# Kernel optimization log

Measured on AMD Instinct MI355X. Metric: run time of the kernel, lower is better.

The kernel has to match this reference:

```python
import jax, jax.numpy as jnp
import numpy as np
import math

B, S, D, H, DFF, V = 8, 512, 512, 8, 2048, 32000
EPS = 1e-5

def _pe_table(max_len, d):
    pos = jnp.arange(max_len, dtype=jnp.float32)[:, None]
    i = jnp.arange(d)
    exponent = (2 * (i // 2)).astype(jnp.float32) / d
    angle = pos / jnp.power(10000.0, exponent)[None, :]
    return jnp.where(i % 2 == 0, jnp.sin(angle), jnp.cos(angle))

def _ln(x, g, b):
    mu = jnp.mean(x, -1, keepdims=True)
    var = jnp.mean((x - mu) ** 2, -1, keepdims=True)
    return g * (x - mu) * jax.lax.rsqrt(var + EPS) + b

def setup_inputs() -> dict:
    key = jax.random.key(0)
    ks = jax.random.split(key, 16)
    n = jax.random.normal
    return {
        "tokens": jax.random.randint(ks[0], (B, S), 0, V, dtype=jnp.int32),
        "emb": n(ks[1], (V, D), jnp.float32),
        "pe": _pe_table(1000, D),
        "Wq": n(ks[2], (H, D, D), jnp.float32), "bq": jnp.zeros((H, D), jnp.float32),
        "Wk": n(ks[3], (H, D, D), jnp.float32), "bk": jnp.zeros((H, D), jnp.float32),
        "Wv": n(ks[4], (H, D, D), jnp.float32), "bv": jnp.zeros((H, D), jnp.float32),
        "Wo": n(ks[5], (H * D, D), jnp.float32), "bo": jnp.zeros((D,), jnp.float32),
        "g1": jnp.ones((D,), jnp.float32), "be1": jnp.zeros((D,), jnp.float32),
        "W1": n(ks[6], (D, DFF), jnp.float32), "b1": jnp.zeros((DFF,), jnp.float32),
        "W2": n(ks[7], (DFF, D), jnp.float32), "b2": jnp.zeros((D,), jnp.float32),
        "g2": jnp.ones((D,), jnp.float32), "be2": jnp.zeros((D,), jnp.float32),
        "Wf": n(ks[8], (D, V), jnp.float32), "bf": jnp.zeros((V,), jnp.float32),
    }

def reference(tokens, emb, pe, Wq, bq, Wk, bk, Wv, bv, Wo, bo, g1, be1,
              W1, b1, W2, b2, g2, be2, Wf, bf):
    x = emb[tokens] + pe[:tokens.shape[1]]  # [B,S,D]
    res = x
    # input-level "causal" mask over (seq, feature) plane, as in the source
    mask = jnp.triu(jnp.ones((S, D), dtype=bool), k=1)
    xm = jnp.where(mask, 0.0, x)
    scale = 1.0 / math.sqrt(D)
    q = jnp.einsum('bsd,hde->hbse', xm, Wq) + bq[:, None, None, :]
    k = jnp.einsum('bsd,hde->hbse', xm, Wk) + bk[:, None, None, :]
    v = jnp.einsum('bsd,hde->hbse', xm, Wv) + bv[:, None, None, :]
    attn = jax.nn.softmax(jnp.einsum('hbse,hbte->hbst', q, k) * scale, axis=-1)
    o = jnp.einsum('hbst,hbte->hbse', attn, v)  # [H,B,S,D]
    cat = o.transpose(1, 2, 0, 3).reshape(B, S, H * D)  # matches torch.cat head order
    x = _ln(res + (cat @ Wo + bo), g1, be1)
    res = x
    ff = jax.nn.relu(x @ W1 + b1) @ W2 + b2
    x = _ln(res + ff, g2, be2)
    return x @ Wf + bf  # [B,S,V]
```

## Files before the change

### kernel.cpp

```cpp
#include <hip/hip_runtime.h>

typedef unsigned short u16;
typedef unsigned int u32;
typedef short s16x8 __attribute__((ext_vector_type(8)));
typedef __bf16 bf16x8 __attribute__((ext_vector_type(8)));
typedef float f32x4 __attribute__((ext_vector_type(4)));

#define DEVI static __device__ __forceinline__

#define SS 512
#define DD 512
#define NFF 2048
#define VV 32000
#define MTOT 4096
#define HD 4096
#define KC 1536

DEVI float bf2f(u16 h){ return __uint_as_float(((u32)h) << 16); }
DEVI u16 f2bf(float f){
  u32 u = __float_as_uint(f);
  return (u16)((u + 0x7FFFu + ((u >> 16) & 1u)) >> 16);
}
DEVI float ldf(const void* p, long i, int isbf){
  return isbf ? bf2f(((const u16*)p)[i]) : ((const float*)p)[i];
}

DEVI f32x4 mfma16(s16x8 a, s16x8 b, f32x4 c){
  return __builtin_amdgcn_mfma_f32_16x16x32_bf16(
      __builtin_bit_cast(bf16x8, a), __builtin_bit_cast(bf16x8, b), c, 0, 0, 0);
}

typedef const __attribute__((address_space(1))) unsigned int* gup;
typedef __attribute__((address_space(3))) unsigned int* lup;
DEVI void gload16(const void* g, void* l){
  __builtin_amdgcn_global_load_lds((gup)g, (lup)l, 16, 0, 0);
}

DEVI float wave_redmax(float v){
  #pragma unroll
  for (int off = 32; off > 0; off >>= 1) v = fmaxf(v, __shfl_xor(v, off, 64));
  return v;
}
DEVI float wave_redsum(float v){
  #pragma unroll
  for (int off = 32; off > 0; off >>= 1) v += __shfl_xor(v, off, 64);
  return v;
}

__global__ void k_dflag(const void* pe, int* flag){
  flag[0] = (*(const u32*)pe == 0x3F800000u) ? 1 : 0;
}

__global__ __launch_bounds__(256) void k_embed(
    const int* __restrict__ tok, const void* __restrict__ emb, const void* __restrict__ pe,
    float* __restrict__ x, u16* __restrict__ xm2, const int* __restrict__ dflag)
{
  int isbf = dflag[0];
  int blk = blockIdx.x;
  int s = blk & (SS - 1);
  int t = tok[blk];
  long rb = (long)blk * 1024;
  for (int d = threadIdx.x; d < DD; d += 256){
    float e = ldf(emb, (long)t * DD + d, isbf) + ldf(pe, (long)s * DD + d, isbf);
    x[(long)blk * DD + d] = e;
    float m = (d <= s) ? e : 0.f;
    u16 hi = f2bf(m);
    u16 lo = f2bf(m - bf2f(hi));
    xm2[rb + d] = hi;
    xm2[rb + 512 + d] = lo;
  }
}

__global__ __launch_bounds__(256) void k_wsplitT(
    const void* __restrict__ Wq, const void* __restrict__ Wk,
    u16* __restrict__ Wq2, u16* __restrict__ Wk2, const int* __restrict__ dflag)
{
  int isbf = dflag[0];
  int zz = blockIdx.z;
  const void* in = (zz < 8) ? Wq : Wk;
  u16* out = (zz < 8) ? Wq2 : Wk2;
  int z = zz & 7;
  long zin = (long)z * DD * DD;
  long zout = (long)z * DD * 1024;
  __shared__ float t[32][33];
  int e0 = blockIdx.x * 32, d0 = blockIdx.y * 32;
  int tx = threadIdx.x & 31, ty = threadIdx.x >> 5;
  #pragma unroll
  for (int i = 0; i < 4; i++){
    int d = ty + i * 8;
    t[d][tx] = ldf(in, zin + (long)(d0 + d) * DD + e0 + tx, isbf);
  }
  __syncthreads();
  #pragma unroll
  for (int i = 0; i < 4; i++){
    int e = ty + i * 8;
    float v = t[tx][e];
    u16 hi = f2bf(v);
    u16 lo = f2bf(v - bf2f(hi));
    long ob = zout + (long)(e0 + e) * 1024 + d0 + tx;
    out[ob] = hi;
    out[ob + 512] = lo;
  }
}

__global__ __launch_bounds__(256) void k_transAll(
    const void* __restrict__ Wv, const void* __restrict__ Wo,
    const void* __restrict__ W1, const void* __restrict__ W2,
    const void* __restrict__ Wf,
    u16* __restrict__ WvT, u16* __restrict__ WoT, u16* __restrict__ W1T,
    u16* __restrict__ W2T, u16* __restrict__ WfT, const int* __restrict__ dflag)
{
  int isbf = dflag[0];
  int f = blockIdx.x;
  const void* in; u16* out; int R, C, gx, loc;
  if (f < 2048)      { in = Wv; out = WvT; R = 512;  C = 512;   gx = 16;   loc = f; }
  else if (f < 4096) { in = Wo; out = WoT; R = 4096; C = 512;   gx = 16;   loc = f - 2048; }
  else if (f < 5120) { in = W1; out = W1T; R = 512;  C = 2048;  gx = 64;   loc = f - 4096; }
  else if (f < 6144) { in = W2; out = W2T; R = 2048; C = 512;   gx = 16;   loc = f - 5120; }
  else               { in = Wf; out = WfT; R = 512;  C = 32000; gx = 1000; loc = f - 6144; }
  int bx = loc % gx;
  int rest = loc / gx;
  int gy = R >> 5;
  int by = rest % gy, z = rest / gy;
  long zo = (long)z * R * C;
  __shared__ float t[32][33];
  int c0 = bx * 32, r0 = by * 32;
  int tx = threadIdx.x & 31, ty = threadIdx.x >> 5;
  #pragma unroll
  for (int i = 0; i < 4; i++){
    int r = ty + i * 8;
    t[r][tx] = ldf(in, zo + (long)(r0 + r) * C + c0 + tx, isbf);
  }
  __syncthreads();
  #pragma unroll
  for (int i = 0; i < 4; i++){
    int c = ty + i * 8;
    out[zo + (long)(c0 + c) * R + r0 + tx] = f2bf(t[tx][c]);
  }
}

enum { EP_QK = 0, EP_SCALE = 1, EP_VT = 2, EP_CAT = 3, EP_OUT = 4,
       EP_F32RES = 5, EP_RELU = 6 };

template<int MODE, bool GSWAP>
__global__ __launch_bounds__(256) void k_mfma(
    const u16* __restrict__ A, long sA, int lda,
    const u16* __restrict__ Bt, long sB,
    void* __restrict__ Cv,
    const void* __restrict__ bias,
    const float* __restrict__ res,
    int K, int ldc, float scale,
    const int* __restrict__ dflag)
{
  int isbf = dflag[0];
  int z = blockIdx.z;
  const u16* Ab = A + (long)z * sA;
  const u16* Bb = Bt + (long)z * sB;
  __shared__ __align__(16) u16 As[2][4][128][8];
  __shared__ __align__(16) u16 Bs[2][4][128][8];
  int m0 = (GSWAP ? blockIdx.x : blockIdx.y) * 128;
  int n0 = (GSWAP ? blockIdx.y : blockIdx.x) * 128;
  int tid = threadIdx.x;
  int lane = tid & 63, w = tid >> 6;
  int wr = (w >> 1) * 64, wc = (w & 1) * 64;
  int l15 = lane & 15, l4 = lane >> 4;
  int s0 = w * 64 + lane;
  int ar0 = s0 & 127, ak0 = s0 >> 7;
  int ak1 = ak0 + 2;
  f32x4 zero = {0.f, 0.f, 0.f, 0.f};
  f32x4 acc[4][4];
  #pragma unroll
  for (int i = 0; i < 4; i++)
    #pragma unroll
    for (int j = 0; j < 4; j++) acc[i][j] = zero;

  const long arow0 = (long)(m0 + ar0) * lda;
  const long brow0 = (long)(n0 + ar0) * K;

  #define STAGE(buf, k0) do{ \
    u16* AsF = &As[buf][0][0][0]; \
    u16* BsF = &Bs[buf][0][0][0]; \
    gload16(Ab + arow0 + (k0) + ak0 * 8, AsF + (long)(w * 64) * 8); \
    gload16(Ab + arow0 + (k0) + ak1 * 8, AsF + (long)(256 + w * 64) * 8); \
    gload16(Bb + brow0 + (k0) + ak0 * 8, BsF + (long)(w * 64) * 8); \
    gload16(Bb + brow0 + (k0) + ak1 * 8, BsF + (long)(256 + w * 64) * 8); \
  }while(0)

  #define COMPUTE(buf) do{ \
    s16x8 af[4], bfr[4]; \
    _Pragma("unroll") \
    for (int i = 0; i < 4; i++) af[i] = *(const s16x8*)&As[buf][l4][wr + i * 16 + l15][0]; \
    _Pragma("unroll") \
    for (int j = 0; j < 4; j++) bfr[j] = *(const s16x8*)&Bs[buf][l4][wc + j * 16 + l15][0]; \
    _Pragma("unroll") \
    for (int i = 0; i < 4; i++) \
      _Pragma("unroll") \
      for (int j = 0; j < 4; j++) \
        acc[i][j] = mfma16(af[i], bfr[j], acc[i][j]); \
  }while(0)

  STAGE(0, 0);
  __syncthreads();
  for (int k0 = 0; k0 < K; k0 += 64){
    STAGE(1, k0 + 32);
    COMPUTE(0);
    __syncthreads();
    if (k0 + 64 < K) STAGE(0, k0 + 64);
    COMPUTE(1);
    __syncthreads();
  }
  #undef STAGE
  #undef COMPUTE

  int mbase = m0 + wr + l4 * 4;
  int nbase = n0 + wc + l15;
  if constexpr (MODE == EP_F32RES){
    float* C = (float*)Cv;
    #pragma unroll
    for (int j = 0; j < 4; j++){
      int n = nbase + j * 16;
      float badd = ldf(bias, n, isbf);
      #pragma unroll
      for (int i = 0; i < 4; i++)
        #pragma unroll
        for (int r = 0; r < 4; r++){
          long a = (long)(mbase + i * 16 + r) * ldc + n;
          C[a] = acc[i][j][r] + badd + res[a];
        }
    }
  } else if constexpr (MODE == EP_RELU){
    u16* C = (u16*)Cv;
    #pragma unroll
    for (int j = 0; j < 4; j++){
      int n = nbase + j * 16;
      float badd = ldf(bias, n, isbf);
      #pragma unroll
      for (int i = 0; i < 4; i++)
        #pragma unroll
        for (int r = 0; r < 4; r++)
          C[(long)(mbase + i * 16 + r) * ldc + n] = f2bf(fmaxf(acc[i][j][r] + badd, 0.f));
    }
  }
}

template<int MODE, bool GSWAP, int AMAP, int BMAP>
__global__ __launch_bounds__(512, 2) void k_mfma2(
    const u16* __restrict__ A, long sA, int lda,
    const u16* __restrict__ Bt, long sB, int ldb,
    void* __restrict__ Cv,
    const void* __restrict__ bias,
    const float* __restrict__ res,
    int K, int ldc, float scale,
    const int* __restrict__ dflag)
{
  int isbf = dflag[0];
  int z = blockIdx.z;
  const u16* Ab = A + (long)z * sA;
  const u16* Bb = Bt + (long)z * sB;
  __shared__ __align__(16) char smem[65536];
  u16* SA = (u16*)smem;
  u16* SB = (u16*)(smem + 32768);
  int m0 = (GSWAP ? blockIdx.x : blockIdx.y) * 256;
  int n0 = (GSWAP ? blockIdx.y : blockIdx.x) * 256;
  int tid = threadIdx.x;
  int lane = tid & 63, w = tid >> 6;
  int wm = (w >> 2) * 128, wn = (w & 3) * 64;
  int l15 = lane & 15, l4 = lane >> 4;
  int row = tid & 255, ob = tid >> 8;
  f32x4 zero = {0.f, 0.f, 0.f, 0.f};
  f32x4 acc[8][4];
  #pragma unroll
  for (int i = 0; i < 8; i++)
    #pragma unroll
    for (int j = 0; j < 4; j++) acc[i][j] = zero;

  const long arow0 = (long)(m0 + row) * lda;
  const long brow0 = (long)(n0 + row) * ldb;

  #define STAGE2(buf, k0_) do{ \
    int ka = (AMAP == 1) ? ((k0_) < 512 ? (k0_) : (k0_) - 512) \
           : (AMAP == 2) ? ((k0_) < 1024 ? (k0_) : (k0_) - 1024) : (k0_); \
    int kb = (BMAP == 1) ? ((k0_) < 512 ? (k0_) : (k0_) - 512) \
           : (BMAP == 2) ? ((k0_) < 1024 ? (k0_) : (k0_) - 1024) : (k0_); \
    gload16(Ab + arow0 + ka + ob * 8,       SA + ((buf) * 8192 + (ob * 256 + row) * 8)); \
    gload16(Ab + arow0 + ka + (ob + 2) * 8, SA + ((buf) * 8192 + ((ob + 2) * 256 + row) * 8)); \
    gload16(Bb + brow0 + kb + ob * 8,       SB + ((buf) * 8192 + (ob * 256 + row) * 8)); \
    gload16(Bb + brow0 + kb + (ob + 2) * 8, SB + ((buf) * 8192 + ((ob + 2) * 256 + row) * 8)); \
  }while(0)

  #define COMPUTE2(buf) do{ \
    s16x8 bfr[4]; \
    _Pragma("unroll") \
    for (int j = 0; j < 4; j++) \
      bfr[j] = *(const s16x8*)(SB + ((buf) * 8192 + l4 * 2048 + (wn + j * 16 + l15) * 8)); \
    _Pragma("unroll") \
    for (int i = 0; i < 8; i++){ \
      s16x8 af = *(const s16x8*)(SA + ((buf) * 8192 + l4 * 2048 + (wm + i * 16 + l15) * 8)); \
      _Pragma("unroll") \
      for (int j = 0; j < 4; j++) \
        acc[i][j] = mfma16(af, bfr[j], acc[i][j]); \
    } \
  }while(0)

  STAGE2(0, 0);
  __syncthreads();
  for (int k0 = 0; k0 < K; k0 += 64){
    STAGE2(1, k0 + 32);
    COMPUTE2(0);
    __syncthreads();
    if (k0 + 64 < K) STAGE2(0, k0 + 64);
    COMPUTE2(1);
    __syncthreads();
  }
  #undef STAGE2
  #undef COMPUTE2

  int mbase = m0 + wm + l4 * 4;
  int nbase = n0 + wn + l15;
  if constexpr (MODE == EP_QK){
    u16* C = (u16*)Cv + (long)z * ((long)MTOT * 1024);
    #pragma unroll
    for (int j = 0; j < 4; j++){
      int n = nbase + j * 16;
      float badd = ldf(bias, (long)z * DD + n, isbf);
      #pragma unroll
      for (int i = 0; i < 8; i++)
        #pragma unroll
        for (int r = 0; r < 4; r++){
          float qv = acc[i][j][r] + badd;
          u16 hi = f2bf(qv);
          u16 lo = f2bf(qv - bf2f(hi));
          long rb = (long)(mbase + i * 16 + r) * 1024;
          C[rb + n] = hi;
          C[rb + 512 + n] = lo;
        }
    }
  } else if constexpr (MODE == EP_SCALE){
    float* C = (float*)Cv + (long)z * SS * SS;
    #pragma unroll
    for (int i = 0; i < 8; i++)
      #pragma unroll
      for (int j = 0; j < 4; j++)
        #pragma unroll
        for (int r = 0; r < 4; r++)
          C[(long)(mbase + i * 16 + r) * SS + nbase + j * 16] = acc[i][j][r] * scale;
  } else if constexpr (MODE == EP_VT){
    u16* C = (u16*)Cv;
    #pragma unroll
    for (int i = 0; i < 8; i++){
      int mrow = mbase + i * 16;
      int b = mrow >> 9, s = mrow & (SS - 1);
      #pragma unroll
      for (int j = 0; j < 4; j++){
        int n = nbase + j * 16;
        float badd = ldf(bias, (long)z * DD + n, isbf);
        ushort4 pk;
        pk.x = f2bf(acc[i][j][0] + badd); pk.y = f2bf(acc[i][j][1] + badd);
        pk.z = f2bf(acc[i][j][2] + badd); pk.w = f2bf(acc[i][j][3] + badd);
        *(ushort4*)&C[((long)(z * 8 + b) * DD + n) * SS + s] = pk;
      }
    }
  } else if constexpr (MODE == EP_CAT){
    u16* C = (u16*)Cv;
    int h = z >> 3, b = z & 7;
    #pragma unroll
    for (int i = 0; i < 8; i++){
      int s = mbase + i * 16;
      #pragma unroll
      for (int j = 0; j < 4; j++){
        int n = nbase + j * 16;
        #pragma unroll
        for (int r = 0; r < 4; r++)
          C[((long)b * SS + s + r) * HD + (long)h * DD + n] = f2bf(acc[i][j][r]);
      }
    }
  } else if constexpr (MODE == EP_OUT){
    float* O = (float*)Cv;
    float* ldsT = (float*)smem;
    const int RST = 260;
    int hs16 = (w >> 2) * 16;
    float badd[4];
    #pragma unroll
    for (int j = 0; j < 4; j++) badd[j] = ldf(bias, n0 + wn + j * 16 + l15, isbf);
    #pragma unroll
    for (int i = 0; i < 8; i++){
      __syncthreads();
      #pragma unroll
      for (int j = 0; j < 4; j++){
        int col = wn + j * 16 + l15;
        #pragma unroll
        for (int r = 0; r < 4; r++)
          ldsT[(hs16 + l4 * 4 + r) * RST + col] = acc[i][j][r] + badd[j];
      }
      __syncthreads();
      #pragma unroll
      for (int p = 0; p < 4; p++){
        int chunk = tid + p * 512;
        int lr = chunk >> 6, c4 = chunk & 63;
        int gm = m0 + (lr >> 4) * 128 + i * 16 + (lr & 15);
        float4 v = *(float4*)&ldsT[lr * RST + c4 * 4];
        *(float4*)&O[(long)gm * ldc + n0 + c4 * 4] = v;
      }
    }
  }
}

__global__ __launch_bounds__(256) void k_softmax(const float* __restrict__ S, u16* __restrict__ P)
{
  int row = blockIdx.x * 4 + (threadIdx.x >> 6);
  int lane = threadIdx.x & 63;
  const float* p = S + (long)row * SS + lane * 8;
  float4 v0 = *(const float4*)p;
  float4 v1 = *(const float4*)(p + 4);
  float v[8] = {v0.x, v0.y, v0.z, v0.w, v1.x, v1.y, v1.z, v1.w};
  float mx = v[0];
  #pragma unroll
  for (int i = 1; i < 8; i++) mx = fmaxf(mx, v[i]);
  mx = wave_redmax(mx);
  float e[8], sum = 0.f;
  #pragma unroll
  for (int i = 0; i < 8; i++){ e[i] = expf(v[i] - mx); sum += e[i]; }
  sum = wave_redsum(sum);
  float inv = 1.f / sum;
  u16* q = P + (long)row * SS + lane * 8;
  ushort4 o0, o1;
  o0.x = f2bf(e[0] * inv); o0.y = f2bf(e[1] * inv);
  o0.z = f2bf(e[2] * inv); o0.w = f2bf(e[3] * inv);
  o1.x = f2bf(e[4] * inv); o1.y = f2bf(e[5] * inv);
  o1.z = f2bf(e[6] * inv); o1.w = f2bf(e[7] * inv);
  *(ushort4*)q = o0;
  *(ushort4*)(q + 4) = o1;
}

template<bool WF32>
__global__ __launch_bounds__(256) void k_ln(
    const float* __restrict__ X, const void* __restrict__ g, const void* __restrict__ be,
    u16* __restrict__ Yb, float* __restrict__ Yf, const int* __restrict__ dflag)
{
  int isbf = dflag[0];
  int row = blockIdx.x * 4 + (threadIdx.x >> 6);
  int lane = threadIdx.x & 63;
  const float* p = X + (long)row * DD + lane * 8;
  float4 v0 = *(const float4*)p;
  float4 v1 = *(const float4*)(p + 4);
  float v[8] = {v0.x, v0.y, v0.z, v0.w, v1.x, v1.y, v1.z, v1.w};
  float s = 0.f;
  #pragma unroll
  for (int i = 0; i < 8; i++) s += v[i];
  s = wave_redsum(s);
  float mu = s * (1.f / DD);
  float d_[8], sq = 0.f;
  #pragma unroll
  for (int i = 0; i < 8; i++){ d_[i] = v[i] - mu; sq += d_[i] * d_[i]; }
  sq = wave_redsum(sq);
  float rs = 1.f / sqrtf(sq * (1.f / DD) + 1e-5f);
  #pragma unroll
  for (int i = 0; i < 8; i++){
    int dd = lane * 8 + i;
    float y = ldf(g, dd, isbf) * d_[i] * rs + ldf(be, dd, isbf);
    Yb[(long)row * DD + dd] = f2bf(y);
    if (WF32) Yf[(long)row * DD + dd] = y;
  }
}

extern "C" void kernel_launch(void* const* d_in, const int* in_sizes, int n_in,
                              void* d_out, int out_size, void* d_ws, size_t ws_size,
                              hipStream_t stream)
{
  const int* tokens = (const int*)d_in[0];
  const void* emb = d_in[1];
  const void* pe  = d_in[2];
  const void* Wq  = d_in[3];
  const void* bq  = d_in[4];
  const void* Wk  = d_in[5];
  const void* bk  = d_in[6];
  const void* Wv  = d_in[7];
  const void* bv  = d_in[8];
  const void* Wo  = d_in[9];
  const void* bo  = d_in[10];
  const void* g1  = d_in[11];
  const void* be1 = d_in[12];
  const void* W1  = d_in[13];
  const void* b1  = d_in[14];
  const void* W2  = d_in[15];
  const void* b2  = d_in[16];
  const void* g2  = d_in[17];
  const void* be2 = d_in[18];
  const void* Wf  = d_in[19];
  const void* bfb = d_in[20];
  float* out = (float*)d_out;
  char* ws = (char*)d_ws;
  char* DO = (char*)d_out;

  const size_t MB = 1ull << 20;
  int* dflag = (int*)ws;
  u16* x2b   = (u16*)(ws + 1 * MB);
  u16* WfT   = (u16*)(ws + 8 * MB);

  float* x    = (float*)(DO + 0 * MB);
  u16*   xm2  = (u16*)(DO + 8 * MB);
  u16*   Wq2  = (u16*)(DO + 16 * MB);
  u16*   Wk2  = (u16*)(DO + 24 * MB);
  u16*   WvT  = (u16*)(DO + 32 * MB);
  u16*   WoT  = (u16*)(DO + 36 * MB);
  u16*   W1T  = (u16*)(DO + 40 * MB);
  u16*   W2T  = (u16*)(DO + 42 * MB);
  u16*   q2   = (u16*)(DO + 48 * MB);
  u16*   k2   = (u16*)(DO + 112 * MB);
  float* sc   = (float*)(DO + 176 * MB);
  u16*   attn = (u16*)(DO + 240 * MB);
  u16*   vT   = (u16*)(DO + 272 * MB);
  u16*   cat  = (u16*)(DO + 304 * MB);
  float* proj = (float*)(DO + 336 * MB);
  float* x1f  = (float*)(DO + 344 * MB);
  u16*   x1b  = (u16*)(DO + 352 * MB);
  u16*   ff1  = (u16*)(DO + 356 * MB);
  float* ff2  = (float*)(DO + 372 * MB);

  const float scale = 0.04419417382415922f;
  const long HSL = 262144;
  const long WSL = 524288;
  const long QSL = 524288;

  k_dflag<<<1, 1, 0, stream>>>(pe, dflag);
  k_embed<<<dim3(4096), 256, 0, stream>>>(tokens, emb, pe, x, xm2, dflag);

  k_wsplitT<<<dim3(16, 16, 16), 256, 0, stream>>>(Wq, Wk, Wq2, Wk2, dflag);
  k_transAll<<<dim3(22144), 256, 0, stream>>>(
      Wv, Wo, W1, W2, Wf, WvT, WoT, W1T, W2T, WfT, dflag);

  k_mfma2<EP_QK, false, 1, 2><<<dim3(2, 16, 8), 512, 0, stream>>>(
      xm2, 0, 1024, Wq2, WSL, 1024, q2, bq, nullptr, KC, 0, 0.f, dflag);
  k_mfma2<EP_QK, false, 1, 2><<<dim3(2, 16, 8), 512, 0, stream>>>(
      xm2, 0, 1024, Wk2, WSL, 1024, k2, bk, nullptr, KC, 0, 0.f, dflag);
  k_mfma2<EP_VT, false, 0, 0><<<dim3(2, 16, 8), 512, 0, stream>>>(
      xm2, 0, 1024, WvT, HSL, 512, vT, bv, nullptr, DD, 0, 0.f, dflag);

  k_mfma2<EP_SCALE, false, 1, 2><<<dim3(2, 2, 64), 512, 0, stream>>>(
      q2, QSL, 1024, k2, QSL, 1024, sc, nullptr, nullptr, KC, 0, scale, dflag);
  k_softmax<<<dim3(8192), 256, 0, stream>>>(sc, attn);

  k_mfma2<EP_CAT, false, 0, 0><<<dim3(2, 2, 64), 512, 0, stream>>>(
      attn, HSL, SS, vT, HSL, 512, cat, nullptr, nullptr, SS, 0, 0.f, dflag);

  k_mfma<EP_F32RES, false><<<dim3(4, 32, 1), 256, 0, stream>>>(
      cat, 0, HD, WoT, 0, proj, bo, x, HD, DD, 0.f, dflag);
  k_ln<true><<<dim3(1024), 256, 0, stream>>>(proj, g1, be1, x1b, x1f, dflag);

  k_mfma<EP_RELU, false><<<dim3(16, 32, 1), 256, 0, stream>>>(
      x1b, 0, DD, W1T, 0, ff1, b1, nullptr, DD, NFF, 0.f, dflag);
  k_mfma<EP_F32RES, false><<<dim3(4, 32, 1), 256, 0, stream>>>(
      ff1, 0, NFF, W2T, 0, ff2, b2, x1f, NFF, DD, 0.f, dflag);
  k_ln<false><<<dim3(1024), 256, 0, stream>>>(ff2, g2, be2, x2b, nullptr, dflag);

  k_mfma2<EP_OUT, true, 0, 0><<<dim3(16, 125, 1), 512, 0, stream>>>(
      x2b, 0, DD, WfT, 0, 512, out, bfb, nullptr, DD, VV, 0.f, dflag);
}
```

Baseline: 1.004 ms.

## Shrink big GEMM tile to 128x256 with 256-thread blocks

Replaces the 512-thread 256x256-tile GEMM kernel with a 256-thread 128x256 variant. Each of the four waves now covers all 128 rows and a 64-column slice, and LDS use drops to 48KB. All launches are updated to double the grid along M. The aim is more blocks and better CU occupancy and load balance on the grids that were small (2x2x64, 2x16x8). The cost is less operand reuse per block and more global traffic for the B operand.

```diff
diff --git a/kernel.cpp b/kernel.cpp
--- a/kernel.cpp
+++ b/kernel.cpp
@@ -244,7 +244,7 @@
 }
 
 template<int MODE, bool GSWAP, int AMAP, int BMAP>
-__global__ __launch_bounds__(512, 2) void k_mfma2(
+__global__ __launch_bounds__(256) void k_mfma3(
     const u16* __restrict__ A, long sA, int lda,
     const u16* __restrict__ Bt, long sB, int ldb,
     void* __restrict__ Cv,
@@ -257,16 +257,16 @@
   int z = blockIdx.z;
   const u16* Ab = A + (long)z * sA;
   const u16* Bb = Bt + (long)z * sB;
-  __shared__ __align__(16) char smem[65536];
+  __shared__ __align__(16) char smem[49152];
   u16* SA = (u16*)smem;
-  u16* SB = (u16*)(smem + 32768);
-  int m0 = (GSWAP ? blockIdx.x : blockIdx.y) * 256;
+  u16* SB = (u16*)(smem + 16384);
+  int m0 = (GSWAP ? blockIdx.x : blockIdx.y) * 128;
   int n0 = (GSWAP ? blockIdx.y : blockIdx.x) * 256;
   int tid = threadIdx.x;
   int lane = tid & 63, w = tid >> 6;
-  int wm = (w >> 2) * 128, wn = (w & 3) * 64;
+  int wn = w * 64;
   int l15 = lane & 15, l4 = lane >> 4;
-  int row = tid & 255, ob = tid >> 8;
+  int arow = tid & 127, akc = tid >> 7;
   f32x4 zero = {0.f, 0.f, 0.f, 0.f};
   f32x4 acc[8][4];
   #pragma unroll
@@ -274,48 +274,50 @@
     #pragma unroll
     for (int j = 0; j < 4; j++) acc[i][j] = zero;
 
-  const long arow0 = (long)(m0 + row) * lda;
-  const long brow0 = (long)(n0 + row) * ldb;
-
-  #define STAGE2(buf, k0_) do{ \
+  const long arow0 = (long)(m0 + arow) * lda;
+  const long brow0 = (long)(n0 + tid) * ldb;
+
+  #define STAGE3(buf, k0_) do{ \
     int ka = (AMAP == 1) ? ((k0_) < 512 ? (k0_) : (k0_) - 512) \
            : (AMAP == 2) ? ((k0_) < 1024 ? (k0_) : (k0_) - 1024) : (k0_); \
     int kb = (BMAP == 1) ? ((k0_) < 512 ? (k0_) : (k0_) - 512) \
            : (BMAP == 2) ? ((k0_) < 1024 ? (k0_) : (k0_) - 1024) : (k0_); \
-    gload16(Ab + arow0 + ka + ob * 8,       SA + ((buf) * 8192 + (ob * 256 + row) * 8)); \
-    gload16(Ab + arow0 + ka + (ob + 2) * 8, SA + ((buf) * 8192 + ((ob + 2) * 256 + row) * 8)); \
-    gload16(Bb + brow0 + kb + ob * 8,       SB + ((buf) * 8192 + (ob * 256 + row) * 8)); \
-    gload16(Bb + brow0 + kb + (ob + 2) * 8, SB + ((buf) * 8192 + ((ob + 2) * 256 + row) * 8)); \
+    gload16(Ab + arow0 + ka + akc * 8,       SA + ((buf) * 4096 + (akc * 128 + arow) * 8)); \
+    gload16(Ab + arow0 + ka + (akc + 2) * 8, SA + ((buf) * 4096 + ((akc + 2) * 128 + arow) * 8)); \
+    gload16(Bb + brow0 + kb + 0,      SB + ((buf) * 8192 + (0 * 256 + tid) * 8)); \
+    gload16(Bb + brow0 + kb + 8,      SB + ((buf) * 8192 + (1 * 256 + tid) * 8)); \
+    gload16(Bb + brow0 + kb + 16,     SB + ((buf) * 8192 + (2 * 256 + tid) * 8)); \
+    gload16(Bb + brow0 + kb + 24,     SB + ((buf) * 8192 + (3 * 256 + tid) * 8)); \
   }while(0)
 
-  #define COMPUTE2(buf) do{ \
+  #define COMPUTE3(buf) do{ \
     s16x8 bfr[4]; \
     _Pragma("unroll") \
     for (int j = 0; j < 4; j++) \
       bfr[j] = *(const s16x8*)(SB + ((buf) * 8192 + l4 * 2048 + (wn + j * 16 + l15) * 8)); \
     _Pragma("unroll") \
     for (int i = 0; i < 8; i++){ \
-      s16x8 af = *(const s16x8*)(SA + ((buf) * 8192 + l4 * 2048 + (wm + i * 16 + l15) * 8)); \
+      s16x8 af = *(const s16x8*)(SA + ((buf) * 4096 + l4 * 1024 + (i * 16 + l15) * 8)); \
       _Pragma("unroll") \
       for (int j = 0; j < 4; j++) \
         acc[i][j] = mfma16(af, bfr[j], acc[i][j]); \
     } \
   }while(0)
 
-  STAGE2(0, 0);
+  STAGE3(0, 0);
   __syncthreads();
   for (int k0 = 0; k0 < K; k0 += 64){
-    STAGE2(1, k0 + 32);
-    COMPUTE2(0);
+    STAGE3(1, k0 + 32);
+    COMPUTE3(0);
     __syncthreads();
-    if (k0 + 64 < K) STAGE2(0, k0 + 64);
-    COMPUTE2(1);
+    if (k0 + 64 < K) STAGE3(0, k0 + 64);
+    COMPUTE3(1);
     __syncthreads();
   }
-  #undef STAGE2
-  #undef COMPUTE2
-
-  int mbase = m0 + wm + l4 * 4;
+  #undef STAGE3
+  #undef COMPUTE3
+
+  int mbase = m0 + l4 * 4;
   int nbase = n0 + wn + l15;
   if constexpr (MODE == EP_QK){
     u16* C = (u16*)Cv + (long)z * ((long)MTOT * 1024);
@@ -378,10 +380,9 @@
     float* O = (float*)Cv;
     float* ldsT = (float*)smem;
     const int RST = 260;
-    int hs16 = (w >> 2) * 16;
     float badd[4];
     #pragma unroll
-    for (int j = 0; j < 4; j++) badd[j] = ldf(bias, n0 + wn + j * 16 + l15, isbf);
+    for (int j = 0; j < 4; j++) badd[j] = ldf(bias, nbase + j * 16, isbf);
     #pragma unroll
     for (int i = 0; i < 8; i++){
       __syncthreads();
@@ -390,14 +391,14 @@
         int col = wn + j * 16 + l15;
         #pragma unroll
         for (int r = 0; r < 4; r++)
-          ldsT[(hs16 + l4 * 4 + r) * RST + col] = acc[i][j][r] + badd[j];
+          ldsT[(l4 * 4 + r) * RST + col] = acc[i][j][r] + badd[j];
       }
       __syncthreads();
       #pragma unroll
       for (int p = 0; p < 4; p++){
-        int chunk = tid + p * 512;
+        int chunk = tid + p * 256;
         int lr = chunk >> 6, c4 = chunk & 63;
-        int gm = m0 + (lr >> 4) * 128 + i * 16 + (lr & 15);
+        int gm = m0 + i * 16 + lr;
         float4 v = *(float4*)&ldsT[lr * RST + c4 * 4];
         *(float4*)&O[(long)gm * ldc + n0 + c4 * 4] = v;
       }
@@ -529,18 +530,18 @@
   k_transAll<<<dim3(22144), 256, 0, stream>>>(
       Wv, Wo, W1, W2, Wf, WvT, WoT, W1T, W2T, WfT, dflag);
 
-  k_mfma2<EP_QK, false, 1, 2><<<dim3(2, 16, 8), 512, 0, stream>>>(
+  k_mfma3<EP_QK, false, 1, 2><<<dim3(2, 32, 8), 256, 0, stream>>>(
       xm2, 0, 1024, Wq2, WSL, 1024, q2, bq, nullptr, KC, 0, 0.f, dflag);
-  k_mfma2<EP_QK, false, 1, 2><<<dim3(2, 16, 8), 512, 0, stream>>>(
+  k_mfma3<EP_QK, false, 1, 2><<<dim3(2, 32, 8), 256, 0, stream>>>(
       xm2, 0, 1024, Wk2, WSL, 1024, k2, bk, nullptr, KC, 0, 0.f, dflag);
-  k_mfma2<EP_VT, false, 0, 0><<<dim3(2, 16, 8), 512, 0, stream>>>(
+  k_mfma3<EP_VT, false, 0, 0><<<dim3(2, 32, 8), 256, 0, stream>>>(
       xm2, 0, 1024, WvT, HSL, 512, vT, bv, nullptr, DD, 0, 0.f, dflag);
 
-  k_mfma2<EP_SCALE, false, 1, 2><<<dim3(2, 2, 64), 512, 0, stream>>>(
+  k_mfma3<EP_SCALE, false, 1, 2><<<dim3(2, 4, 64), 256, 0, stream>>>(
       q2, QSL, 1024, k2, QSL, 1024, sc, nullptr, nullptr, KC, 0, scale, dflag);
   k_softmax<<<dim3(8192), 256, 0, stream>>>(sc, attn);
 
-  k_mfma2<EP_CAT, false, 0, 0><<<dim3(2, 2, 64), 512, 0, stream>>>(
+  k_mfma3<EP_CAT, false, 0, 0><<<dim3(2, 4, 64), 256, 0, stream>>>(
       attn, HSL, SS, vT, HSL, 512, cat, nullptr, nullptr, SS, 0, 0.f, dflag);
 
   k_mfma<EP_F32RES, false><<<dim3(4, 32, 1), 256, 0, stream>>>(
@@ -553,6 +554,6 @@
       ff1, 0, NFF, W2T, 0, ff2, b2, x1f, NFF, DD, 0.f, dflag);
   k_ln<false><<<dim3(1024), 256, 0, stream>>>(ff2, g2, be2, x2b, nullptr, dflag);
 
-  k_mfma2<EP_OUT, true, 0, 0><<<dim3(16, 125, 1), 512, 0, stream>>>(
+  k_mfma3<EP_OUT, true, 0, 0><<<dim3(32, 125, 1), 256, 0, stream>>>(
       x2b, 0, DD, WfT, 0, 512, out, bfb, nullptr, DD, VV, 0.f, dflag);
 }
```

Result: slower. 1.239 ms (+23.5%).

## Fuse QK^T score GEMM with row softmax into a single kernel

Applied to the files above, without the earlier changes.

Replaces the score GEMM (which wrote fp32 scores to global memory) plus the separate softmax kernel with one kernel. Each block computes a 128-row by 512-column score tile, then does the row max and sum reductions in registers and LDS and writes bf16 probabilities directly. This removes the fp32 score round trip through memory and one launch. In exchange the grid shrinks from 256 blocks to 256 blocks with a different shape (each block now covers full rows with an 8-wave N split and smaller A tiles), and it adds extra syncs and a reduction epilogue.

```diff
diff --git a/kernel.cpp b/kernel.cpp
--- a/kernel.cpp
+++ b/kernel.cpp
@@ -36,11 +36,6 @@
   __builtin_amdgcn_global_load_lds((gup)g, (lup)l, 16, 0, 0);
 }
 
-DEVI float wave_redmax(float v){
-  #pragma unroll
-  for (int off = 32; off > 0; off >>= 1) v = fmaxf(v, __shfl_xor(v, off, 64));
-  return v;
-}
 DEVI float wave_redsum(float v){
   #pragma unroll
   for (int off = 32; off > 0; off >>= 1) v += __shfl_xor(v, off, 64);
@@ -335,15 +330,6 @@
           C[rb + 512 + n] = lo;
         }
     }
-  } else if constexpr (MODE == EP_SCALE){
-    float* C = (float*)Cv + (long)z * SS * SS;
-    #pragma unroll
-    for (int i = 0; i < 8; i++)
-      #pragma unroll
-      for (int j = 0; j < 4; j++)
-        #pragma unroll
-        for (int r = 0; r < 4; r++)
-          C[(long)(mbase + i * 16 + r) * SS + nbase + j * 16] = acc[i][j][r] * scale;
   } else if constexpr (MODE == EP_VT){
     u16* C = (u16*)Cv;
     #pragma unroll
@@ -405,31 +391,137 @@
   }
 }
 
-__global__ __launch_bounds__(256) void k_softmax(const float* __restrict__ S, u16* __restrict__ P)
-{
-  int row = blockIdx.x * 4 + (threadIdx.x >> 6);
-  int lane = threadIdx.x & 63;
-  const float* p = S + (long)row * SS + lane * 8;
-  float4 v0 = *(const float4*)p;
-  float4 v1 = *(const float4*)(p + 4);
-  float v[8] = {v0.x, v0.y, v0.z, v0.w, v1.x, v1.y, v1.z, v1.w};
-  float mx = v[0];
-  #pragma unroll
-  for (int i = 1; i < 8; i++) mx = fmaxf(mx, v[i]);
-  mx = wave_redmax(mx);
-  float e[8], sum = 0.f;
-  #pragma unroll
-  for (int i = 0; i < 8; i++){ e[i] = expf(v[i] - mx); sum += e[i]; }
-  sum = wave_redsum(sum);
-  float inv = 1.f / sum;
-  u16* q = P + (long)row * SS + lane * 8;
-  ushort4 o0, o1;
-  o0.x = f2bf(e[0] * inv); o0.y = f2bf(e[1] * inv);
-  o0.z = f2bf(e[2] * inv); o0.w = f2bf(e[3] * inv);
-  o1.x = f2bf(e[4] * inv); o1.y = f2bf(e[5] * inv);
-  o1.z = f2bf(e[6] * inv); o1.w = f2bf(e[7] * inv);
-  *(ushort4*)q = o0;
-  *(ushort4*)(q + 4) = o1;
+template<int AMAP, int BMAP>
+__global__ __launch_bounds__(512, 2) void k_fsm(
+    const u16* __restrict__ A, long sA, int lda,
+    const u16* __restrict__ Bt, long sB, int ldb,
+    u16* __restrict__ P, int K, float scale,
+    const int* __restrict__ dflag)
+{
+  int z = blockIdx.z;
+  const u16* Ab = A + (long)z * sA;
+  const u16* Bb = Bt + (long)z * sB;
+  __shared__ __align__(16) char smem[81920];
+  u16* SA = (u16*)smem;
+  u16* SB = (u16*)(smem + 16384);
+  int m0 = blockIdx.x * 128;
+  int tid = threadIdx.x;
+  int lane = tid & 63, w = tid >> 6;
+  int wn = w * 64;
+  int l15 = lane & 15, l4 = lane >> 4;
+  f32x4 zero = {0.f, 0.f, 0.f, 0.f};
+  f32x4 acc[8][4];
+  #pragma unroll
+  for (int i = 0; i < 8; i++)
+    #pragma unroll
+    for (int j = 0; j < 4; j++) acc[i][j] = zero;
+
+  const long arow0 = (long)(m0 + (tid & 127)) * lda;
+  const int akc = tid >> 7;
+  const long brow0 = (long)tid * ldb;
+
+  #define STAGEF(buf, k0_) do{ \
+    int ka = (AMAP == 1) ? ((k0_) < 512 ? (k0_) : (k0_) - 512) \
+           : (AMAP == 2) ? ((k0_) < 1024 ? (k0_) : (k0_) - 1024) : (k0_); \
+    int kb = (BMAP == 1) ? ((k0_) < 512 ? (k0_) : (k0_) - 512) \
+           : (BMAP == 2) ? ((k0_) < 1024 ? (k0_) : (k0_) - 1024) : (k0_); \
+    gload16(Ab + arow0 + ka + akc * 8, SA + ((buf) * 4096 + tid * 8)); \
+    gload16(Bb + brow0 + kb + 0,  SB + ((buf) * 16384 + (0 * 512 + tid) * 8)); \
+    gload16(Bb + brow0 + kb + 8,  SB + ((buf) * 16384 + (1 * 512 + tid) * 8)); \
+    gload16(Bb + brow0 + kb + 16, SB + ((buf) * 16384 + (2 * 512 + tid) * 8)); \
+    gload16(Bb + brow0 + kb + 24, SB + ((buf) * 16384 + (3 * 512 + tid) * 8)); \
+  }while(0)
+
+  #define COMPUTEF(buf) do{ \
+    s16x8 bfr[4]; \
+    _Pragma("unroll") \
+    for (int j = 0; j < 4; j++) \
+      bfr[j] = *(const s16x8*)(SB + ((buf) * 16384 + l4 * 4096 + (wn + j * 16 + l15) * 8)); \
+    _Pragma("unroll") \
+    for (int i = 0; i < 8; i++){ \
+      s16x8 af = *(const s16x8*)(SA + ((buf) * 4096 + l4 * 1024 + (i * 16 + l15) * 8)); \
+      _Pragma("unroll") \
+      for (int j = 0; j < 4; j++) \
+        acc[i][j] = mfma16(af, bfr[j], acc[i][j]); \
+    } \
+  }while(0)
+
+  STAGEF(0, 0);
+  __syncthreads();
+  for (int k0 = 0; k0 < K; k0 += 64){
+    STAGEF(1, k0 + 32);
+    COMPUTEF(0);
+    __syncthreads();
+    if (k0 + 64 < K) STAGEF(0, k0 + 64);
+    COMPUTEF(1);
+    __syncthreads();
+  }
+  #undef STAGEF
+  #undef COMPUTEF
+
+  float* sred = (float*)smem;
+  float* srow = (float*)(smem + 4096);
+
+  #pragma unroll
+  for (int i = 0; i < 8; i++)
+    #pragma unroll
+    for (int j = 0; j < 4; j++)
+      acc[i][j] *= scale;
+
+  #pragma unroll
+  for (int i = 0; i < 8; i++)
+    #pragma unroll
+    for (int r = 0; r < 4; r++){
+      float m = fmaxf(fmaxf(acc[i][0][r], acc[i][1][r]),
+                      fmaxf(acc[i][2][r], acc[i][3][r]));
+      #pragma unroll
+      for (int off = 1; off < 16; off <<= 1) m = fmaxf(m, __shfl_xor(m, off, 64));
+      if (l15 == 0) sred[w * 128 + l4 * 4 + i * 16 + r] = m;
+    }
+  __syncthreads();
+  if (tid < 128){
+    float m = sred[tid];
+    #pragma unroll
+    for (int w2 = 1; w2 < 8; w2++) m = fmaxf(m, sred[w2 * 128 + tid]);
+    srow[tid] = m;
+  }
+  __syncthreads();
+  #pragma unroll
+  for (int i = 0; i < 8; i++)
+    #pragma unroll
+    for (int r = 0; r < 4; r++){
+      float rm = srow[l4 * 4 + i * 16 + r];
+      float s = 0.f;
+      #pragma unroll
+      for (int j = 0; j < 4; j++){
+        float e = expf(acc[i][j][r] - rm);
+        acc[i][j][r] = e;
+        s += e;
+      }
+      #pragma unroll
+      for (int off = 1; off < 16; off <<= 1) s += __shfl_xor(s, off, 64);
+      if (l15 == 0) sred[w * 128 + l4 * 4 + i * 16 + r] = s;
+    }
+  __syncthreads();
+  if (tid < 128){
+    float s = 0.f;
+    #pragma unroll
+    for (int w2 = 0; w2 < 8; w2++) s += sred[w2 * 128 + tid];
+    srow[tid] = 1.f / s;
+  }
+  __syncthreads();
+  u16* Pz = P + (long)z * ((long)SS * SS);
+  #pragma unroll
+  for (int i = 0; i < 8; i++)
+    #pragma unroll
+    for (int r = 0; r < 4; r++){
+      int rl = l4 * 4 + i * 16 + r;
+      float inv = srow[rl];
+      long rb = (long)(m0 + rl) * SS;
+      #pragma unroll
+      for (int j = 0; j < 4; j++)
+        Pz[rb + wn + j * 16 + l15] = f2bf(acc[i][j][r] * inv);
+    }
 }
 
 template<bool WF32>
@@ -507,7 +599,6 @@
   u16*   W2T  = (u16*)(DO + 42 * MB);
   u16*   q2   = (u16*)(DO + 48 * MB);
   u16*   k2   = (u16*)(DO + 112 * MB);
-  float* sc   = (float*)(DO + 176 * MB);
   u16*   attn = (u16*)(DO + 240 * MB);
   u16*   vT   = (u16*)(DO + 272 * MB);
   u16*   cat  = (u16*)(DO + 304 * MB);
@@ -536,9 +627,8 @@
   k_mfma2<EP_VT, false, 0, 0><<<dim3(2, 16, 8), 512, 0, stream>>>(
       xm2, 0, 1024, WvT, HSL, 512, vT, bv, nullptr, DD, 0, 0.f, dflag);
 
-  k_mfma2<EP_SCALE, false, 1, 2><<<dim3(2, 2, 64), 512, 0, stream>>>(
-      q2, QSL, 1024, k2, QSL, 1024, sc, nullptr, nullptr, KC, 0, scale, dflag);
-  k_softmax<<<dim3(8192), 256, 0, stream>>>(sc, attn);
+  k_fsm<1, 2><<<dim3(4, 1, 64), 512, 0, stream>>>(
+      q2, QSL, 1024, k2, QSL, 1024, attn, KC, scale, dflag);
 
   k_mfma2<EP_CAT, false, 0, 0><<<dim3(2, 2, 64), 512, 0, stream>>>(
       attn, HSL, SS, vT, HSL, 512, cat, nullptr, nullptr, SS, 0, 0.f, dflag);
```

After: 1.019 ms. About the same (+1.6%).
